# Optimization experiments

Measured on AMD Instinct MI355X. Metric: run time of the kernel, lower is better.

Reference implementation:

```python
import jax, jax.numpy as jnp
import numpy as np

V, WD, H, B, S, A = 50000, 300, 300, 64, 128, 8
H2 = 2 * H
NEG = -1e9


def _reverse_padded(x, lens):
    # reverse each sequence within its valid length; zeros elsewhere
    T = x.shape[1]
    idx = lens[:, None] - 1 - jnp.arange(T)[None, :]          # [B,T]
    valid = (idx >= 0)
    idx = jnp.clip(idx, 0, T - 1)
    return jnp.take_along_axis(x, idx[:, :, None], axis=1) * valid[:, :, None]


def _lstm_dir(x, lens, Wih, Whh, bih, bhh):
    # single-direction LSTM; emulates pack_padded: state frozen and output 0 past lens
    Bn, T, _ = x.shape
    Hn = Whh.shape[1]
    h0 = jnp.zeros((Bn, Hn), x.dtype)
    valid = (jnp.arange(T)[None, :] < lens[:, None]).astype(x.dtype)  # [B,T]

    def step(carry, inp):
        h, c = carry
        xt, vt = inp                                          # xt [B,D], vt [B,1]
        g = xt @ Wih.T + bih + h @ Whh.T + bhh                # [B,4H]
        i, f, gg, o = jnp.split(g, 4, axis=-1)                # torch gate order i,f,g,o
        i = jax.nn.sigmoid(i); f = jax.nn.sigmoid(f)
        o = jax.nn.sigmoid(o); gg = jnp.tanh(gg)
        c_new = f * c + i * gg
        h_new = o * jnp.tanh(c_new)
        h = vt * h_new + (1.0 - vt) * h
        c = vt * c_new + (1.0 - vt) * c
        return (h, c), vt * h_new

    _, outs = jax.lax.scan(step, (h0, h0), (x.transpose(1, 0, 2), valid.T[:, :, None]))
    return outs.transpose(1, 0, 2)                            # [B,T,H]


def _bilstm(x, lens, Wih, Whh, bih, bhh):
    fwd = _lstm_dir(x, lens, Wih[0], Whh[0], bih[0], bhh[0])
    xr = _reverse_padded(x, lens)
    bwd = _lstm_dir(xr, lens, Wih[1], Whh[1], bih[1], bhh[1])
    bwd = _reverse_padded(bwd, lens)
    return jnp.concatenate([fwd, bwd], axis=-1)               # [B,T,2H]


def setup_inputs() -> dict:
    key = jax.random.key(0)
    ks = jax.random.split(key, 16)
    lens_t = jax.random.randint(ks[0], (B,), S // 2, S + 1)
    ids_t = jax.random.randint(ks[1], (B, S), 1, V)
    text = jnp.where(jnp.arange(S)[None, :] < lens_t[:, None], ids_t, 0)
    lens_a = jax.random.randint(ks[2], (B,), 2, A + 1)
    ids_a = jax.random.randint(ks[3], (B, A), 1, V)
    aspect_ids = jnp.where(jnp.arange(A)[None, :] < lens_a[:, None], ids_a, 0)
    position_weight = jax.random.uniform(ks[4], (B, S), jnp.float32) * (text != 0)
    s = 0.05
    emb = jax.random.normal(ks[5], (V, WD), jnp.float32) * s
    emb = emb.at[0].set(0.0)  # padding row

    def lstm_params(k):
        k1, k2, k3, k4 = jax.random.split(k, 4)
        return (jax.random.normal(k1, (2, 4 * H, WD), jnp.float32) * s,
                jax.random.normal(k2, (2, 4 * H, H), jnp.float32) * s,
                jax.random.normal(k3, (2, 4 * H), jnp.float32) * s,
                jax.random.normal(k4, (2, 4 * H), jnp.float32) * s)

    l1_Wih, l1_Whh, l1_bih, l1_bhh = lstm_params(ks[6])
    l2_Wih, l2_Whh, l2_bih, l2_bhh = lstm_params(ks[7])
    return dict(
        text=text, aspect_ids=aspect_ids, position_weight=position_weight, emb=emb,
        l1_Wih=l1_Wih, l1_Whh=l1_Whh, l1_bih=l1_bih, l1_bhh=l1_bhh,
        l2_Wih=l2_Wih, l2_Whh=l2_Whh, l2_bih=l2_bih, l2_bhh=l2_bhh,
        lin1_W=jax.random.normal(ks[8], (2, H2, 2 * H2), jnp.float32) * s,
        lin1_b=jax.random.normal(ks[9], (2, H2), jnp.float32) * s,
        lin2_W=jax.random.normal(ks[10], (2, 1, H2), jnp.float32) * s,
        lin2_b=jax.random.normal(ks[11], (2, 1), jnp.float32) * s,
        fc_W=jax.random.normal(ks[12], (3, H2), jnp.float32) * s,
        fc_b=jax.random.normal(ks[13], (3,), jnp.float32) * s,
    )


def reference(text, aspect_ids, position_weight, emb,
              l1_Wih, l1_Whh, l1_bih, l1_bhh,
              l2_Wih, l2_Whh, l2_bih, l2_bhh,
              lin1_W, lin1_b, lin2_W, lin2_b, fc_W, fc_b):
    text_len = jnp.sum(text != 0, axis=-1)
    asp_len = jnp.sum(aspect_ids != 0, axis=-1)
    masks = (text != 0).astype(jnp.float32)          # [B,S]
    tmasks = (aspect_ids != 0).astype(jnp.float32)   # [B,A]
    wf = emb[text]                                    # [B,S,WD]
    af = emb[aspect_ids]                              # [B,A,WD]
    v = _bilstm(wf, text_len, l1_Wih, l1_Whh, l1_bih, l1_bhh)   # [B,S,2H]
    e = _bilstm(af, asp_len, l2_Wih, l2_Whh, l2_bih, l2_bhh)    # [B,A,2H]
    pair_mask = masks[:, :, None] * tmasks[:, None, :]          # [B,S,A]
    for i in range(2):
        a = jnp.einsum('bsd,bad->bsa', v, e)
        a = jnp.where(pair_mask == 0, NEG, a)
        a = jax.nn.softmax(a, axis=2)
        mid = jnp.einsum('bsa,bad->bsd', a, e)                  # [B,S,2H]
        mid = jnp.concatenate([mid, v], axis=-1)                # [B,S,4H]
        mid = jax.nn.leaky_relu(mid @ lin1_W[i].T + lin1_b[i])  # [B,S,2H]
        t = jax.nn.sigmoid(v @ lin2_W[i].T + lin2_b[i])         # [B,S,1]
        v = (1.0 - t) * mid + t * v
        v = position_weight[:, :, None] * v
    e_masked = jnp.where(tmasks[:, :, None] == 0, NEG, e)
    query = jnp.max(e_masked, axis=1)                           # [B,2H]
    alpha = jnp.einsum('bsd,bd->bs', v, query)
    alpha = jnp.where(masks == 0, NEG, alpha)
    alpha = jax.nn.softmax(alpha, axis=1)
    z = jnp.einsum('bs,bsd->bd', alpha, v)                      # [B,2H]
    return z @ fc_W.T + fc_b                                    # [B,3]
```

## Files before the change

### kernel.cpp

```cpp
#include <hip/hip_runtime.h>
#include <hip/hip_bf16.h>
#include <hip/hip_fp16.h>


typedef unsigned short u16;
typedef __attribute__((ext_vector_type(8))) short short8;
typedef __attribute__((ext_vector_type(4))) float floatx4;

#define NEGV -1e9f
#define MFMA __builtin_amdgcn_mfma_f32_16x16x32_bf16

__device__ __forceinline__ float bf2f(u16 u) {
    union { unsigned int i; float f; } x; x.i = ((unsigned int)u) << 16; return x.f;
}
__device__ __forceinline__ u16 f2bf(float f) {
    unsigned int u = __float_as_uint(f);
    unsigned int r = (u + 0x7fff + ((u >> 16) & 1)) >> 16;
    return (u16)r;
}
__device__ __forceinline__ float h16(u16 u) {
    __half h; *(u16*)&h = u; return __half2float(h);
}
__device__ __forceinline__ u16 f16(float f) {
    __half h = __float2half(f); return *(u16*)&h;
}
__device__ __forceinline__ float sigm(float x) { return 1.f / (1.f + expf(-x)); }
__device__ __forceinline__ float rdf(const void* p, size_t i, int flag) {
    return flag ? ((const float*)p)[i] : bf2f(((const u16*)p)[i]);
}

#if defined(__has_builtin)
# if __has_builtin(__builtin_amdgcn_fdot2)
#  define USE_FDOT2_BUILTIN 1
# endif
#endif
typedef __attribute__((ext_vector_type(2))) _Float16 half2v;
__device__ __forceinline__ float dot2f(unsigned int w, unsigned int h, float acc) {
#ifdef USE_FDOT2_BUILTIN
    union { unsigned int u; half2v v; } a, b;
    a.u = w; b.u = h;
    return __builtin_amdgcn_fdot2(a.v, b.v, acc, false);
#else
    asm("v_dot2_f32_f16 %0, %1, %2, %0" : "+v"(acc) : "v"(w), "v"(h));
    return acc;
#endif
}

__global__ void k_detect(const void* __restrict__ emb, int* __restrict__ flag) {
    __shared__ int cnt;
    if (threadIdx.x == 0) cnt = 0;
    __syncthreads();
    u16 x = ((const u16*)emb)[4096 + threadIdx.x];
    int e = (x >> 7) & 0xFF;
    if (e >= 0x8A) atomicAdd(&cnt, 1);
    __syncthreads();
    if (threadIdx.x == 0) *flag = (cnt > 8) ? 1 : 0;
}

__global__ void k_prep_small(const int* __restrict__ text, const int* __restrict__ asp,
                             int* __restrict__ lens) {
    int tid = threadIdx.x;
    if (tid < 64) {
        int c = 0;
        for (int s = 0; s < 128; ++s) c += (text[tid * 128 + s] != 0);
        lens[tid] = c;
    } else if (tid < 128) {
        int b = tid - 64; int c = 0;
        for (int a = 0; a < 8; ++a) c += (asp[b * 8 + a] != 0);
        lens[64 + b] = c;
    }
}

__global__ void k_pad_wih2(const void* __restrict__ W1, const void* __restrict__ W2,
                           const int* __restrict__ flag,
                           u16* __restrict__ d1h, u16* __restrict__ d1l,
                           u16* __restrict__ d2h, u16* __restrict__ d2l) {
    int i = blockIdx.x * 256 + threadIdx.x;
    if (i >= 2 * 2432 * 320) return;
    int f = *flag;
    int layer = i / (2432 * 320), r = i - layer * (2432 * 320);
    int n = r / 320, k = r - n * 320;
    const void* W = layer ? W2 : W1;
    float val = (n < 2400 && k < 300) ? rdf(W, (size_t)n * 300 + k, f) : 0.f;
    u16 hi = f2bf(val);
    float lo = val - bf2f(hi);
    if (layer) { d2h[r] = hi; d2l[r] = f2bf(lo); }
    else       { d1h[r] = hi; d1l[r] = f2bf(lo); }
}

__global__ void k_whhT2(const void* __restrict__ W1, const void* __restrict__ W2,
                        const int* __restrict__ flag,
                        u16* __restrict__ d1, u16* __restrict__ d2) {
    int i = blockIdx.x * 256 + threadIdx.x;
    if (i >= 2 * 720000) return;
    int f = *flag;
    int layer = i / 720000, r = i - layer * 720000;
    int dir = r / 360000, rr = r - dir * 360000;
    int kp = rr / 2400, t = rr - kp * 2400;
    int cc = t >> 1, j = t & 1;
    int k = 2 * kp + j;
    const void* W = layer ? W2 : W1;
    u16 bits = f16(rdf(W, (size_t)dir * 360000 + (size_t)cc * 300 + k, f));
    if (layer) d2[r] = bits; else d1[r] = bits;
}

__global__ void k_pad_lin1AB(const void* __restrict__ W, const int* __restrict__ flag,
                             u16* __restrict__ Ahi, u16* __restrict__ Alo,
                             u16* __restrict__ Bhi, u16* __restrict__ Blo) {
    int i = blockIdx.x * 256 + threadIdx.x;
    if (i >= 2 * 640 * 608) return;
    int f = *flag;
    int it = i / (640 * 608), r = i - it * (640 * 608);
    int n = r / 608, k = r - n * 608;
    float va = 0.f, vb = 0.f;
    if (n < 600 && k < 600) {
        va = rdf(W, (size_t)it * 720000 + (size_t)n * 1200 + k, f);
        vb = rdf(W, (size_t)it * 720000 + (size_t)n * 1200 + 600 + k, f);
    }
    u16 h;
    h = f2bf(va); Ahi[i] = h; Alo[i] = f2bf(va - bf2f(h));
    h = f2bf(vb); Bhi[i] = h; Blo[i] = f2bf(vb - bf2f(h));
}

__global__ void k_esplit(const float* __restrict__ e,
                         u16* __restrict__ ehi, u16* __restrict__ elo) {
    int i = blockIdx.x * 256 + threadIdx.x;
    if (i >= 512 * 608) return;
    int r = i / 608, k = i - r * 608;
    float val = (k < 600) ? e[r * 600 + k] : 0.f;
    u16 h = f2bf(val);
    ehi[i] = h;
    elo[i] = f2bf(val - bf2f(h));
}

__global__ void k_small(const void* pw, const void* l2w, const void* l2b,
                        const void* fcw, const void* fcb, const void* lb,
                        const void* b1i, const void* b1h, const void* b2i, const void* b2h,
                        const int* __restrict__ flag,
                        float* __restrict__ dst, float* __restrict__ bl,
                        float* __restrict__ bt, float* __restrict__ ba) {
    int i = blockIdx.x * 256 + threadIdx.x;
    int f = *flag;
    if (i < 8192)            dst[i] = rdf(pw, i, f);
    else if (i < 9392)       dst[i] = rdf(l2w, i - 8192, f);
    else if (i < 9394)       dst[i] = rdf(l2b, i - 9392, f);
    else if (i < 11194)      dst[i] = rdf(fcw, i - 9394, f);
    else if (i < 11197)      dst[i] = rdf(fcb, i - 11194, f);
    if (i < 1280) {
        int dir = i / 640, c = i - dir * 640;
        bl[i] = (c < 600) ? rdf(lb, dir * 600 + c, f) : 0.f;
    }
    if (i < 2400) {
        bt[i] = rdf(b1i, i, f) + rdf(b1h, i, f);
        ba[i] = rdf(b2i, i, f) + rdf(b2h, i, f);
    }
}

__device__ __forceinline__ void gemm_emb_tile(
    const void* __restrict__ emb, const int* __restrict__ ids,
    int base, int rpb, int stride, int f,
    const u16* __restrict__ Bhi, const u16* __restrict__ Blo,
    const float* __restrict__ bias,
    u16* __restrict__ C, int ldc, int nstore, int bx, int by, int tid)
{
    int wave = tid >> 6, lane = tid & 63;
    int l15 = lane & 15, quad = lane >> 4;
    int m0 = bx * 64 + wave * 16;
    int n0 = by * 64;

    int m = m0 + l15;
    int b = m / rpb, j = m - b * rpb;
    int id = ids[b * stride + base + j];
    const float* arow_f = (const float*)emb + (size_t)id * 300;
    const u16*   arow_b = (const u16*)emb + (size_t)id * 300;

    const u16* Bp  = Bhi + (size_t)(n0 + l15) * 320 + quad * 8;
    const u16* Bp2 = Blo + (size_t)(n0 + l15) * 320 + quad * 8;

    floatx4 acc0 = {0.f, 0.f, 0.f, 0.f};
    floatx4 acc1 = acc0, acc2 = acc0, acc3 = acc0;

    for (int kc = 0; kc < 10; ++kc) {
        int ko = kc * 32 + quad * 8;
        short8 ahi, alo;
        if (f) {
            if (ko + 8 <= 300) {
                float4 fa = *(const float4*)(arow_f + ko);
                float4 fb = *(const float4*)(arow_f + ko + 4);
                float vv[8] = {fa.x, fa.y, fa.z, fa.w, fb.x, fb.y, fb.z, fb.w};
                #pragma unroll
                for (int t = 0; t < 8; ++t) {
                    u16 h = f2bf(vv[t]);
                    ahi[t] = (short)h;
                    alo[t] = (short)f2bf(vv[t] - bf2f(h));
                }
            } else {
                #pragma unroll
                for (int t = 0; t < 8; ++t) {
                    int k = ko + t;
                    float vv = (k < 300) ? arow_f[k] : 0.f;
                    u16 h = f2bf(vv);
                    ahi[t] = (short)h;
                    alo[t] = (short)f2bf(vv - bf2f(h));
                }
            }
        } else {
            #pragma unroll
            for (int t = 0; t < 8; ++t) {
                int k = ko + t;
                ahi[t] = (k < 300) ? (short)arow_b[k] : (short)0;
                alo[t] = 0;
            }
        }
        int ko2 = kc * 32;
        short8 bh0 = *(const short8*)(Bp + ko2);
        short8 bh1 = *(const short8*)(Bp + (size_t)16 * 320 + ko2);
        short8 bh2 = *(const short8*)(Bp + (size_t)32 * 320 + ko2);
        short8 bh3 = *(const short8*)(Bp + (size_t)48 * 320 + ko2);
        short8 bl0 = *(const short8*)(Bp2 + ko2);
        short8 bl1 = *(const short8*)(Bp2 + (size_t)16 * 320 + ko2);
        short8 bl2 = *(const short8*)(Bp2 + (size_t)32 * 320 + ko2);
        short8 bl3 = *(const short8*)(Bp2 + (size_t)48 * 320 + ko2);
        acc0 = MFMA(ahi, bh0, acc0, 0, 0, 0);
        acc1 = MFMA(ahi, bh1, acc1, 0, 0, 0);
        acc2 = MFMA(ahi, bh2, acc2, 0, 0, 0);
        acc3 = MFMA(ahi, bh3, acc3, 0, 0, 0);
        acc0 = MFMA(ahi, bl0, acc0, 0, 0, 0);
        acc1 = MFMA(ahi, bl1, acc1, 0, 0, 0);
        acc2 = MFMA(ahi, bl2, acc2, 0, 0, 0);
        acc3 = MFMA(ahi, bl3, acc3, 0, 0, 0);
        acc0 = MFMA(alo, bh0, acc0, 0, 0, 0);
        acc1 = MFMA(alo, bh1, acc1, 0, 0, 0);
        acc2 = MFMA(alo, bh2, acc2, 0, 0, 0);
        acc3 = MFMA(alo, bh3, acc3, 0, 0, 0);
    }

    #pragma unroll
    for (int c = 0; c < 4; ++c) {
        floatx4 acc = (c == 0) ? acc0 : (c == 1) ? acc1 : (c == 2) ? acc2 : acc3;
        int col = n0 + c * 16 + l15;
        if (col >= nstore) continue;
        float bb = bias[col];
        #pragma unroll
        for (int r = 0; r < 4; ++r) {
            int row = m0 + quad * 4 + r;
            C[(size_t)row * ldc + col] = f16(acc[r] + bb);
        }
    }
}

__global__ __launch_bounds__(256) void gemm_embk(
    const void* __restrict__ emb, const int* __restrict__ ids,
    int base, int rpb, int stride, const int* __restrict__ flag,
    const u16* __restrict__ Bhi, const u16* __restrict__ Blo,
    const float* __restrict__ bias,
    u16* __restrict__ C, int ldc, int nstore)
{
    gemm_emb_tile(emb, ids, base, rpb, stride, *flag, Bhi, Blo, bias,
                  C, ldc, nstore, blockIdx.x, blockIdx.y, threadIdx.x);
}

__device__ __forceinline__ void gemm_core(
    const u16* __restrict__ Ap, const u16* __restrict__ Ap2,
    const u16* __restrict__ Bp, const u16* __restrict__ Bp2,
    int lda, int ldb, int nk,
    floatx4& acc0, floatx4& acc1, floatx4& acc2, floatx4& acc3)
{
    for (int kc = 0; kc < nk; ++kc) {
        int ko = kc * 32;
        short8 bh0 = *(const short8*)(Bp + ko);
        short8 bh1 = *(const short8*)(Bp + (size_t)16 * ldb + ko);
        short8 bh2 = *(const short8*)(Bp + (size_t)32 * ldb + ko);
        short8 bh3 = *(const short8*)(Bp + (size_t)48 * ldb + ko);
        short8 bl0 = *(const short8*)(Bp2 + ko);
        short8 bl1 = *(const short8*)(Bp2 + (size_t)16 * ldb + ko);
        short8 bl2 = *(const short8*)(Bp2 + (size_t)32 * ldb + ko);
        short8 bl3 = *(const short8*)(Bp2 + (size_t)48 * ldb + ko);
        short8 a  = *(const short8*)(Ap + ko);
        short8 al = *(const short8*)(Ap2 + ko);
        acc0 = MFMA(a, bh0, acc0, 0, 0, 0);
        acc1 = MFMA(a, bh1, acc1, 0, 0, 0);
        acc2 = MFMA(a, bh2, acc2, 0, 0, 0);
        acc3 = MFMA(a, bh3, acc3, 0, 0, 0);
        acc0 = MFMA(a, bl0, acc0, 0, 0, 0);
        acc1 = MFMA(a, bl1, acc1, 0, 0, 0);
        acc2 = MFMA(a, bl2, acc2, 0, 0, 0);
        acc3 = MFMA(a, bl3, acc3, 0, 0, 0);
        acc0 = MFMA(al, bh0, acc0, 0, 0, 0);
        acc1 = MFMA(al, bh1, acc1, 0, 0, 0);
        acc2 = MFMA(al, bh2, acc2, 0, 0, 0);
        acc3 = MFMA(al, bh3, acc3, 0, 0, 0);
    }
}

__global__ __launch_bounds__(256) void gemm_ew(
    const u16* __restrict__ Ahi, const u16* __restrict__ Alo,
    const u16* __restrict__ l1a_hi, const u16* __restrict__ l1a_lo,
    float* __restrict__ EW)
{
    int tid = threadIdx.x;
    int wave = tid >> 6, lane = tid & 63;
    int l15 = lane & 15, quad = lane >> 4;
    int iter = blockIdx.z;
    int m0 = blockIdx.x * 64 + wave * 16;
    int n0 = blockIdx.y * 64;
    const u16* Ap  = Ahi + (size_t)(m0 + l15) * 608 + quad * 8;
    const u16* Ap2 = Alo + (size_t)(m0 + l15) * 608 + quad * 8;
    const u16* Bp  = l1a_hi + (size_t)iter * 640 * 608 + (size_t)(n0 + l15) * 608 + quad * 8;
    const u16* Bp2 = l1a_lo + (size_t)iter * 640 * 608 + (size_t)(n0 + l15) * 608 + quad * 8;
    floatx4 acc0 = {0.f, 0.f, 0.f, 0.f};
    floatx4 acc1 = acc0, acc2 = acc0, acc3 = acc0;
    gemm_core(Ap, Ap2, Bp, Bp2, 608, 608, 19, acc0, acc1, acc2, acc3);
    #pragma unroll
    for (int c = 0; c < 4; ++c) {
        floatx4 acc = (c == 0) ? acc0 : (c == 1) ? acc1 : (c == 2) ? acc2 : acc3;
        int col = n0 + c * 16 + l15;
        if (col >= 600) continue;
        #pragma unroll
        for (int r = 0; r < 4; ++r) {
            int row = m0 + quad * 4 + r;
            EW[((size_t)iter * 512 + row) * 600 + col] = acc[r];
        }
    }
}

__global__ __launch_bounds__(256) void gemm_vt(
    const u16* __restrict__ vhi, const u16* __restrict__ vlo,
    const u16* __restrict__ Bhi, const u16* __restrict__ Blo,
    const float* __restrict__ bias,
    const float* __restrict__ EW, const float* __restrict__ a_sm,
    const float* __restrict__ tg, const float* __restrict__ pw,
    float* __restrict__ vio)
{
    __shared__ float al_s[64][8];
    __shared__ float ew_s[8][64];
    int tid = threadIdx.x;
    int wave = tid >> 6, lane = tid & 63;
    int l15 = lane & 15, quad = lane >> 4;
    int m0 = blockIdx.x * 64 + wave * 16;
    int n0 = blockIdx.y * 64;
    int row0 = blockIdx.x * 64;
    int bidx = row0 >> 7;

    for (int i = tid; i < 512; i += 256)
        al_s[i >> 3][i & 7] = a_sm[(size_t)(row0 + (i >> 3)) * 8 + (i & 7)];
    for (int i = tid; i < 512; i += 256) {
        int a = i >> 6, cc = i & 63;
        int col = n0 + cc;
        ew_s[a][cc] = (col < 600) ? EW[((size_t)bidx * 8 + a) * 600 + col] : 0.f;
    }
    __syncthreads();

    const u16* Ap  = vhi + (size_t)(m0 + l15) * 608 + quad * 8;
    const u16* Ap2 = vlo + (size_t)(m0 + l15) * 608 + quad * 8;
    const u16* Bp  = Bhi + (size_t)(n0 + l15) * 608 + quad * 8;
    const u16* Bp2 = Blo + (size_t)(n0 + l15) * 608 + quad * 8;
    floatx4 acc0 = {0.f, 0.f, 0.f, 0.f};
    floatx4 acc1 = acc0, acc2 = acc0, acc3 = acc0;
    gemm_core(Ap, Ap2, Bp, Bp2, 608, 608, 19, acc0, acc1, acc2, acc3);

    #pragma unroll
    for (int c = 0; c < 4; ++c) {
        floatx4 acc = (c == 0) ? acc0 : (c == 1) ? acc1 : (c == 2) ? acc2 : acc3;
        int cc = c * 16 + l15;
        int col = n0 + cc;
        if (col >= 600) continue;
        float bb = bias[col];
        #pragma unroll
        for (int r = 0; r < 4; ++r) {
            int rr = wave * 16 + quad * 4 + r;
            int row = row0 + rr;
            float mid = 0.f;
            #pragma unroll
            for (int a = 0; a < 8; ++a) mid += al_s[rr][a] * ew_s[a][cc];
            float val = acc[r] + bb + mid;
            val = val > 0.f ? val : 0.01f * val;
            float t = tg[row];
            size_t vi = (size_t)row * 600 + col;
            float vv = vio[vi];
            vio[vi] = pw[row] * ((1.f - t) * val + t * vv);
        }
    }
}

__global__ __launch_bounds__(960, 1) void k_lstm6(
    const u16* __restrict__ xf, const u16* __restrict__ xb, int ldx, int rpb,
    int base_f, int base_b, const u16* __restrict__ whhT,
    const int* __restrict__ lens, float* __restrict__ out, int T, int init,
    float* __restrict__ hst, float* __restrict__ cst, int nsteps,
    const u16* __restrict__ xa, const u16* __restrict__ whhA,
    const int* __restrict__ lensA, float* __restrict__ outA,
    float* __restrict__ hstA, float* __restrict__ cstA, int nLstm,
    const void* __restrict__ emb, const int* __restrict__ text,
    int bf_next, int bb_next, const int* __restrict__ flag,
    const u16* __restrict__ wih_hi, const u16* __restrict__ wih_lo,
    const float* __restrict__ bias_t,
    u16* __restrict__ xf_next, u16* __restrict__ xb_next)
{
    __shared__ float part[6][1200];
    __shared__ u16 wlds[6][4][2400];
    __shared__ __align__(4) u16 hs16[304];
    int blk = blockIdx.x;
    if (blk >= nLstm) {
        if (threadIdx.x >= 256) return;
        int g = blk - nLstm;
        int dirn = g / 608; int t = g - dirn * 608;
        int bx = t & 31, by = t >> 5;
        gemm_emb_tile(emb, text, dirn ? bb_next : bf_next, 32, 128, *flag,
                      wih_hi + (dirn ? 1200ull * 320 : 0),
                      wih_lo + (dirn ? 1200ull * 320 : 0),
                      bias_t + (dirn ? 1200 : 0),
                      dirn ? xb_next : xf_next, 1200, 1200, bx, by, threadIdx.x);
        return;
    }
    if (blk >= 128) {
        blk -= 128;
        xf = xa; xb = xa + 1200; ldx = 2400; rpb = 8;
        base_f = 0; base_b = 0;
        whhT = whhA; lens = lensA; out = outA; T = 8; init = 1;
        hst = hstA; cst = cstA; nsteps = 8;
    }
    int tid = threadIdx.x;
    int g6 = tid / 160, u = tid - g6 * 160;
    bool act = (u < 150);
    int b = blk >> 1, dir = blk & 1;
    int len = lens[b];
    float c = 0.f, hf = 0.f;
    const u16* wbase = whhT + (size_t)dir * 360000 + (size_t)g6 * 60000 + 16 * u;

    uint4 wA[8], wB[8];
    if (act) {
        #pragma unroll
        for (int r = 0; r < 8; ++r) {
            wA[r] = *(const uint4*)(wbase + (size_t)r * 2400);
            wB[r] = *(const uint4*)(wbase + (size_t)r * 2400 + 8);
        }
        #pragma unroll
        for (int r = 0; r < 4; ++r) {
            *(uint4*)&wlds[g6][r][16 * u]     = *(const uint4*)(wbase + (size_t)(8 + r) * 2400);
            *(uint4*)&wlds[g6][r][16 * u + 8] = *(const uint4*)(wbase + (size_t)(8 + r) * 2400 + 8);
        }
    }
    if (tid < 300) {
        hf = init ? 0.f : hst[(size_t)blk * 300 + tid];
        c  = init ? 0.f : cst[(size_t)blk * 300 + tid];
        hs16[tid] = f16(hf);
    }
    __syncthreads();
    const u16* wstream = wbase + (size_t)12 * 2400;

    for (int s = 0; s < nsteps; ++s) {
        int pos = dir ? (base_b + nsteps - 1 - s) : (base_f + s);
        if (pos >= len) continue;
        if (act) {
            float a0 = 0.f, a1 = 0.f, a2 = 0.f, a3 = 0.f;
            float a4 = 0.f, a5 = 0.f, a6 = 0.f, a7 = 0.f;
            const unsigned int* h2p = (const unsigned int*)(hs16 + g6 * 50);
            #define DOT8(va, vb, hh)                                   \
                a0 = dot2f((va).x, hh, a0); a1 = dot2f((va).y, hh, a1);\
                a2 = dot2f((va).z, hh, a2); a3 = dot2f((va).w, hh, a3);\
                a4 = dot2f((vb).x, hh, a4); a5 = dot2f((vb).y, hh, a5);\
                a6 = dot2f((vb).z, hh, a6); a7 = dot2f((vb).w, hh, a7);
            #pragma unroll
            for (int r = 0; r < 8; ++r) {
                unsigned int h2 = h2p[r];
                DOT8(wA[r], wB[r], h2);
            }
            #pragma unroll
            for (int r = 0; r < 4; ++r) {
                unsigned int h2 = h2p[8 + r];
                uint4 va = *(const uint4*)&wlds[g6][r][16 * u];
                uint4 vb = *(const uint4*)&wlds[g6][r][16 * u + 8];
                DOT8(va, vb, h2);
            }
            const u16* wp = wstream;
            #pragma unroll 4
            for (int i = 0; i < 13; ++i) {
                unsigned int h2 = h2p[12 + i];
                uint4 va = *(const uint4*)wp;
                uint4 vb = *(const uint4*)(wp + 8);
                wp += 2400;
                DOT8(va, vb, h2);
            }
            #undef DOT8
            float* pp = &part[g6][8 * u];
            float4 w0 = {a0, a1, a2, a3};
            float4 w1 = {a4, a5, a6, a7};
            *(float4*)pp = w0;
            *(float4*)(pp + 4) = w1;
        }
        __syncthreads();
        if (tid < 300) {
            const u16* xr = dir ? (xb + (size_t)(b * rpb + pos - base_b) * ldx)
                                : (xf + (size_t)(b * rpb + pos - base_f) * ldx);
            float gi = h16(xr[tid]), gf = h16(xr[300 + tid]);
            float gg = h16(xr[600 + tid]), go = h16(xr[900 + tid]);
            #pragma unroll
            for (int g = 0; g < 6; ++g) {
                gi += part[g][tid];
                gf += part[g][300 + tid];
                gg += part[g][600 + tid];
                go += part[g][900 + tid];
            }
            gi = sigm(gi); gf = sigm(gf); gg = tanhf(gg); go = sigm(go);
            c = gf * c + gi * gg;
            float hn = go * tanhf(c);
            out[((size_t)b * T + pos) * 600 + dir * 300 + tid] = hn;
            hf = hn;
            hs16[tid] = f16(hn);
        }
        __syncthreads();
    }
    if (tid < 300) {
        hst[(size_t)blk * 300 + tid] = hf;
        cst[(size_t)blk * 300 + tid] = c;
    }
}

__global__ __launch_bounds__(128) void k_scorev(
    const float* __restrict__ v, const float* __restrict__ e,
    const int* __restrict__ text, const int* __restrict__ asp,
    const float* __restrict__ l2w, const float* __restrict__ l2b, int iter,
    float* __restrict__ a_sm, float* __restrict__ tg,
    u16* __restrict__ vhi, u16* __restrict__ vlo)
{
    __shared__ float vs[600];
    __shared__ float red[2][9];
    int row = blockIdx.x;
    int b = row >> 7;
    int t = threadIdx.x, wv = t >> 6, lane = t & 63;
    const float* vrow = v + (size_t)row * 600;
    const float* eb = e + (size_t)b * 4800;
    const float* w2 = l2w + iter * 600;

    for (int d = t; d < 600; d += 128) vs[d] = vrow[d];
    __syncthreads();

    float acc[9];
    #pragma unroll
    for (int j = 0; j < 9; ++j) acc[j] = 0.f;
    for (int d = t; d < 600; d += 128) {
        float vv = vs[d];
        #pragma unroll
        for (int a = 0; a < 8; ++a) acc[a] += vv * eb[a * 600 + d];
        acc[8] += vv * w2[d];
    }
    #pragma unroll
    for (int off = 32; off >= 1; off >>= 1) {
        #pragma unroll
        for (int j = 0; j < 9; ++j) acc[j] += __shfl_down(acc[j], off, 64);
    }
    if (lane == 0) {
        #pragma unroll
        for (int j = 0; j < 9; ++j) red[wv][j] = acc[j];
    }
    __syncthreads();
    if (t == 0) {
        float dots[9];
        #pragma unroll
        for (int j = 0; j < 9; ++j) dots[j] = red[0][j] + red[1][j];
        tg[row] = sigm(dots[8] + l2b[iter]);
        bool sm = (text[row] != 0);
        float sc[8]; float mx = -INFINITY;
        #pragma unroll
        for (int a = 0; a < 8; ++a) {
            sc[a] = (sm && asp[b * 8 + a] != 0) ? dots[a] : NEGV;
            mx = fmaxf(mx, sc[a]);
        }
        float den = 0.f;
        #pragma unroll
        for (int a = 0; a < 8; ++a) { sc[a] = expf(sc[a] - mx); den += sc[a]; }
        float inv = 1.f / den;
        #pragma unroll
        for (int a = 0; a < 8; ++a) a_sm[(size_t)row * 8 + a] = sc[a] * inv;
    }
    for (int d = t; d < 608; d += 128) {
        float val = (d < 600) ? vs[d] : 0.f;
        u16 h = f2bf(val);
        vhi[(size_t)row * 608 + d] = h;
        vlo[(size_t)row * 608 + d] = f2bf(val - bf2f(h));
    }
}

__global__ void k_query(const float* __restrict__ e, const int* __restrict__ asp,
                        float* __restrict__ q) {
    int i = blockIdx.x * 256 + threadIdx.x;
    if (i >= 64 * 600) return;
    int b = i / 600, d = i - b * 600;
    float m = NEGV;
    for (int a = 0; a < 8; ++a)
        if (asp[b * 8 + a] != 0) m = fmaxf(m, e[(size_t)b * 4800 + a * 600 + d]);
    q[i] = m;
}

__global__ __launch_bounds__(128) void k_final(
    const float* __restrict__ v, const float* __restrict__ q,
    const int* __restrict__ text, const float* __restrict__ fcW,
    const float* __restrict__ fcb, const int* __restrict__ flag, void* __restrict__ outv)
{
    __shared__ float red[128];
    __shared__ float al[128];
    __shared__ float zz[600];
    int b = blockIdx.x, s = threadIdx.x;
    const float* vrow = v + (size_t)(b * 128 + s) * 600;
    const float* qb = q + (size_t)b * 600;
    float sc = 0.f;
    for (int d = 0; d < 600; ++d) sc += vrow[d] * qb[d];
    if (text[b * 128 + s] == 0) sc = NEGV;
    red[s] = sc; __syncthreads();
    for (int off = 64; off >= 1; off >>= 1) {
        if (s < off) red[s] = fmaxf(red[s], red[s + off]);
        __syncthreads();
    }
    float mx = red[0]; __syncthreads();
    float ex = expf(sc - mx);
    red[s] = ex; __syncthreads();
    for (int off = 64; off >= 1; off >>= 1) {
        if (s < off) red[s] += red[s + off];
        __syncthreads();
    }
    float alpha = ex / red[0];
    al[s] = alpha; __syncthreads();
    for (int d = s; d < 600; d += 128) {
        float z = 0.f;
        for (int s2 = 0; s2 < 128; ++s2) z += al[s2] * v[(size_t)(b * 128 + s2) * 600 + d];
        zz[d] = z;
    }
    __syncthreads();
    if (s < 3) {
        float o = 0.f;
        for (int d = 0; d < 600; ++d) o += zz[d] * fcW[s * 600 + d];
        o += fcb[s];
        if (*flag) ((float*)outv)[b * 3 + s] = o;
        else       ((u16*)outv)[b * 3 + s] = f2bf(o);
    }
}

extern "C" void kernel_launch(void* const* d_in, const int* in_sizes, int n_in,
                              void* d_out, int out_size, void* d_ws, size_t ws_size,
                              hipStream_t stream) {
    const int*  text   = (const int*)d_in[0];
    const int*  asp    = (const int*)d_in[1];
    const void* pw     = d_in[2];
    const void* emb    = d_in[3];
    const void* l1_Wih = d_in[4];
    const void* l1_Whh = d_in[5];
    const void* l1_bih = d_in[6];
    const void* l1_bhh = d_in[7];
    const void* l2_Wih = d_in[8];
    const void* l2_Whh = d_in[9];
    const void* l2_bih = d_in[10];
    const void* l2_bhh = d_in[11];
    const void* lin1_W = d_in[12];
    const void* lin1_b = d_in[13];
    const void* lin2_W = d_in[14];
    const void* lin2_b = d_in[15];
    const void* fcW    = d_in[16];
    const void* fcb    = d_in[17];
    (void)ws_size; (void)n_in; (void)in_sizes; (void)out_size;

    char* w = (char*)d_ws;
    size_t off = 0;
    auto alloc = [&](size_t bytes) -> void* {
        void* p = w + off;
        off += (bytes + 255) & ~(size_t)255;
        return p;
    };
    int*   flag     = (int*)  alloc(4);
    int*   lens     = (int*)  alloc(128ull * 4);
    float* bias_t   = (float*)alloc(2400ull * 4);
    float* bias_a   = (float*)alloc(2400ull * 4);
    float* bias_l1  = (float*)alloc(1280ull * 4);
    float* smallf   = (float*)alloc(11197ull * 4);
    float* tg       = (float*)alloc(8192ull * 4);
    float* a_sm     = (float*)alloc(8192ull * 8 * 4);
    float* query    = (float*)alloc(64ull * 600 * 4);
    float* hst_t    = (float*)alloc(128ull * 300 * 4);
    float* cst_t    = (float*)alloc(128ull * 300 * 4);
    float* hst_a    = (float*)alloc(128ull * 300 * 4);
    float* cst_a    = (float*)alloc(128ull * 300 * 4);
    float* e        = (float*)alloc(512ull * 600 * 4);
    float* v        = (float*)alloc(8192ull * 600 * 4);
    float* pw_f     = smallf;
    float* l2w_f    = smallf + 8192;
    float* l2b_f    = smallf + 9392;
    float* fcW_f    = smallf + 9394;
    float* fcb_f    = smallf + 11194;
    size_t phase_off = off;
    u16*   wiht_hi  = (u16*)  alloc(2432ull * 320 * 2);
    u16*   wiht_lo  = (u16*)  alloc(2432ull * 320 * 2);
    u16*   wiha_hi  = (u16*)  alloc(2432ull * 320 * 2);
    u16*   wiha_lo  = (u16*)  alloc(2432ull * 320 * 2);
    u16*   whhT_t   = (u16*)  alloc(720000ull * 2);
    u16*   whhT_a   = (u16*)  alloc(720000ull * 2);
    u16*   xf0      = (u16*)  alloc(2048ull * 1200 * 2);
    u16*   xb0      = (u16*)  alloc(2048ull * 1200 * 2);
    u16*   xf1      = (u16*)  alloc(2048ull * 1200 * 2);
    u16*   xb1      = (u16*)  alloc(2048ull * 1200 * 2);
    u16*   xproj_a  = (u16*)  alloc(512ull * 2400 * 2);
    off = phase_off;
    u16*   l1a_hi   = (u16*)  alloc(2ull * 640 * 608 * 2);
    u16*   l1a_lo   = (u16*)  alloc(2ull * 640 * 608 * 2);
    u16*   l1b_hi   = (u16*)  alloc(2ull * 640 * 608 * 2);
    u16*   l1b_lo   = (u16*)  alloc(2ull * 640 * 608 * 2);
    u16*   ehi      = (u16*)  alloc(512ull * 608 * 2);
    u16*   elo      = (u16*)  alloc(512ull * 608 * 2);
    float* EW       = (float*)alloc(2ull * 512 * 600 * 4);
    u16*   vhi      = (u16*)  alloc(8192ull * 608 * 2);
    u16*   vlo      = (u16*)  alloc(8192ull * 608 * 2);

    hipMemsetAsync(v, 0, 8192ull * 600 * 4, stream);
    hipMemsetAsync(e, 0, 512ull * 600 * 4, stream);

    k_detect<<<1, 256, 0, stream>>>(emb, flag);
    k_prep_small<<<1, 128, 0, stream>>>(text, asp, lens);
    k_pad_wih2<<<(2 * 2432 * 320 + 255) / 256, 256, 0, stream>>>(
        l1_Wih, l2_Wih, flag, wiht_hi, wiht_lo, wiha_hi, wiha_lo);
    k_whhT2<<<(2 * 720000 + 255) / 256, 256, 0, stream>>>(
        l1_Whh, l2_Whh, flag, whhT_t, whhT_a);
    k_small<<<49, 256, 0, stream>>>(pw, lin2_W, lin2_b, fcW, fcb, lin1_b,
                                    l1_bih, l1_bhh, l2_bih, l2_bhh, flag,
                                    smallf, bias_l1, bias_t, bias_a);

    gemm_embk<<<dim3(8, 38), 256, 0, stream>>>(emb, asp, 0, 8, 8, flag,
        wiha_hi, wiha_lo, bias_a, xproj_a, 2400, 2400);
    gemm_embk<<<dim3(32, 19), 256, 0, stream>>>(emb, text, 0, 32, 128, flag,
        wiht_hi, wiht_lo, bias_t, xf0, 1200, 1200);
    gemm_embk<<<dim3(32, 19), 256, 0, stream>>>(emb, text, 96, 32, 128, flag,
        wiht_hi + 1200ull * 320, wiht_lo + 1200ull * 320, bias_t + 1200,
        xb0, 1200, 1200);

    for (int kk = 0; kk < 4; ++kk) {
        int bf = 32 * kk;
        int bb = 96 - 32 * kk;
        u16* xfc = (kk & 1) ? xf1 : xf0;
        u16* xbc = (kk & 1) ? xb1 : xb0;
        u16* xfn = (kk & 1) ? xf0 : xf1;
        u16* xbn = (kk & 1) ? xb0 : xb1;
        int nLstm = (kk == 0) ? 256 : 128;
        int haveNext = (kk < 3);
        int nblk = nLstm + (haveNext ? 1216 : 0);
        k_lstm6<<<nblk, 960, 0, stream>>>(xfc, xbc, 1200, 32, bf, bb,
            whhT_t, lens, v, 128, kk == 0 ? 1 : 0, hst_t, cst_t, 32,
            xproj_a, whhT_a, lens + 64, e, hst_a, cst_a, nLstm,
            emb, text, bf + 32, bb - 32, flag, wiht_hi, wiht_lo, bias_t,
            xfn, xbn);
    }

    k_pad_lin1AB<<<(2 * 640 * 608 + 255) / 256, 256, 0, stream>>>(
        lin1_W, flag, l1a_hi, l1a_lo, l1b_hi, l1b_lo);
    k_esplit<<<(512 * 608 + 255) / 256, 256, 0, stream>>>(e, ehi, elo);
    gemm_ew<<<dim3(8, 10, 2), 256, 0, stream>>>(ehi, elo, l1a_hi, l1a_lo, EW);

    for (int iter = 0; iter < 2; ++iter) {
        k_scorev<<<8192, 128, 0, stream>>>(v, e, text, asp, l2w_f, l2b_f,
            iter, a_sm, tg, vhi, vlo);
        gemm_vt<<<dim3(128, 10), 256, 0, stream>>>(vhi, vlo,
            l1b_hi + (size_t)iter * 640 * 608, l1b_lo + (size_t)iter * 640 * 608,
            bias_l1 + iter * 640, EW + (size_t)iter * 512 * 600,
            a_sm, tg, pw_f, v);
    }

    k_query<<<150, 256, 0, stream>>>(e, asp, query);
    k_final<<<64, 128, 0, stream>>>(v, query, text, fcW_f, fcb_f, flag, d_out);
}
```

Measured before the change: 1.102 ms.

## Merge prep kernels and fold query/lin1 padding into LSTM launches

Folds the weight-prep kernels into one large launch, merges the three embedding GEMMs into one grid, and appends the query max-reduction and lin1 weight padding as extra blocks of the LSTM chunk launches. The aim is to cut kernel launch count and fill idle CUs during the latency-bound LSTM recurrence. k_final also stages v tiles through shared memory so the per-row dot product reads coalesced. The risk is that the extra 960-thread blocks compete with the LSTM blocks for CUs. The query blocks run in the kk==1 launch and read the aspect outputs, which depends on the aspect LSTM having finished in an earlier chunk.

```diff
diff --git a/kernel.cpp b/kernel.cpp
--- a/kernel.cpp
+++ b/kernel.cpp
@@ -57,102 +57,68 @@
     if (threadIdx.x == 0) *flag = (cnt > 8) ? 1 : 0;
 }
 
-__global__ void k_prep_small(const int* __restrict__ text, const int* __restrict__ asp,
-                             int* __restrict__ lens) {
+__global__ __launch_bounds__(256) void k_prep_all(
+    const int* __restrict__ text, const int* __restrict__ asp,
+    int* __restrict__ lens, const int* __restrict__ flag,
+    const void* __restrict__ W1ih, const void* __restrict__ W2ih,
+    u16* __restrict__ d1h, u16* __restrict__ d1l,
+    u16* __restrict__ d2h, u16* __restrict__ d2l,
+    const void* __restrict__ W1hh, const void* __restrict__ W2hh,
+    u16* __restrict__ dh1, u16* __restrict__ dh2,
+    const void* pw, const void* l2w, const void* l2b,
+    const void* fcw, const void* fcb, const void* lb,
+    const void* b1i, const void* b1h, const void* b2i, const void* b2h,
+    float* __restrict__ dst, float* __restrict__ bl,
+    float* __restrict__ bt, float* __restrict__ ba)
+{
+    int blk = blockIdx.x;
     int tid = threadIdx.x;
-    if (tid < 64) {
-        int c = 0;
-        for (int s = 0; s < 128; ++s) c += (text[tid * 128 + s] != 0);
-        lens[tid] = c;
-    } else if (tid < 128) {
-        int b = tid - 64; int c = 0;
-        for (int a = 0; a < 8; ++a) c += (asp[b * 8 + a] != 0);
-        lens[64 + b] = c;
-    }
-}
-
-__global__ void k_pad_wih2(const void* __restrict__ W1, const void* __restrict__ W2,
-                           const int* __restrict__ flag,
-                           u16* __restrict__ d1h, u16* __restrict__ d1l,
-                           u16* __restrict__ d2h, u16* __restrict__ d2l) {
-    int i = blockIdx.x * 256 + threadIdx.x;
-    if (i >= 2 * 2432 * 320) return;
     int f = *flag;
-    int layer = i / (2432 * 320), r = i - layer * (2432 * 320);
-    int n = r / 320, k = r - n * 320;
-    const void* W = layer ? W2 : W1;
-    float val = (n < 2400 && k < 300) ? rdf(W, (size_t)n * 300 + k, f) : 0.f;
-    u16 hi = f2bf(val);
-    float lo = val - bf2f(hi);
-    if (layer) { d2h[r] = hi; d2l[r] = f2bf(lo); }
-    else       { d1h[r] = hi; d1l[r] = f2bf(lo); }
-}
-
-__global__ void k_whhT2(const void* __restrict__ W1, const void* __restrict__ W2,
-                        const int* __restrict__ flag,
-                        u16* __restrict__ d1, u16* __restrict__ d2) {
-    int i = blockIdx.x * 256 + threadIdx.x;
-    if (i >= 2 * 720000) return;
-    int f = *flag;
-    int layer = i / 720000, r = i - layer * 720000;
-    int dir = r / 360000, rr = r - dir * 360000;
-    int kp = rr / 2400, t = rr - kp * 2400;
-    int cc = t >> 1, j = t & 1;
-    int k = 2 * kp + j;
-    const void* W = layer ? W2 : W1;
-    u16 bits = f16(rdf(W, (size_t)dir * 360000 + (size_t)cc * 300 + k, f));
-    if (layer) d2[r] = bits; else d1[r] = bits;
-}
-
-__global__ void k_pad_lin1AB(const void* __restrict__ W, const int* __restrict__ flag,
-                             u16* __restrict__ Ahi, u16* __restrict__ Alo,
-                             u16* __restrict__ Bhi, u16* __restrict__ Blo) {
-    int i = blockIdx.x * 256 + threadIdx.x;
-    if (i >= 2 * 640 * 608) return;
-    int f = *flag;
-    int it = i / (640 * 608), r = i - it * (640 * 608);
-    int n = r / 608, k = r - n * 608;
-    float va = 0.f, vb = 0.f;
-    if (n < 600 && k < 600) {
-        va = rdf(W, (size_t)it * 720000 + (size_t)n * 1200 + k, f);
-        vb = rdf(W, (size_t)it * 720000 + (size_t)n * 1200 + 600 + k, f);
-    }
-    u16 h;
-    h = f2bf(va); Ahi[i] = h; Alo[i] = f2bf(va - bf2f(h));
-    h = f2bf(vb); Bhi[i] = h; Blo[i] = f2bf(vb - bf2f(h));
-}
-
-__global__ void k_esplit(const float* __restrict__ e,
-                         u16* __restrict__ ehi, u16* __restrict__ elo) {
-    int i = blockIdx.x * 256 + threadIdx.x;
-    if (i >= 512 * 608) return;
-    int r = i / 608, k = i - r * 608;
-    float val = (k < 600) ? e[r * 600 + k] : 0.f;
-    u16 h = f2bf(val);
-    ehi[i] = h;
-    elo[i] = f2bf(val - bf2f(h));
-}
-
-__global__ void k_small(const void* pw, const void* l2w, const void* l2b,
-                        const void* fcw, const void* fcb, const void* lb,
-                        const void* b1i, const void* b1h, const void* b2i, const void* b2h,
-                        const int* __restrict__ flag,
-                        float* __restrict__ dst, float* __restrict__ bl,
-                        float* __restrict__ bt, float* __restrict__ ba) {
-    int i = blockIdx.x * 256 + threadIdx.x;
-    int f = *flag;
-    if (i < 8192)            dst[i] = rdf(pw, i, f);
-    else if (i < 9392)       dst[i] = rdf(l2w, i - 8192, f);
-    else if (i < 9394)       dst[i] = rdf(l2b, i - 9392, f);
-    else if (i < 11194)      dst[i] = rdf(fcw, i - 9394, f);
-    else if (i < 11197)      dst[i] = rdf(fcb, i - 11194, f);
-    if (i < 1280) {
-        int dir = i / 640, c = i - dir * 640;
-        bl[i] = (c < 600) ? rdf(lb, dir * 600 + c, f) : 0.f;
-    }
-    if (i < 2400) {
-        bt[i] = rdf(b1i, i, f) + rdf(b1h, i, f);
-        ba[i] = rdf(b2i, i, f) + rdf(b2h, i, f);
+    if (blk < 6080) {
+        int i = blk * 256 + tid;
+        int layer = i / (2432 * 320), r = i - layer * (2432 * 320);
+        int n = r / 320, k = r - n * 320;
+        const void* W = layer ? W2ih : W1ih;
+        float val = (n < 2400 && k < 300) ? rdf(W, (size_t)n * 300 + k, f) : 0.f;
+        u16 hi = f2bf(val);
+        float lo = val - bf2f(hi);
+        if (layer) { d2h[r] = hi; d2l[r] = f2bf(lo); }
+        else       { d1h[r] = hi; d1l[r] = f2bf(lo); }
+    } else if (blk < 11705) {
+        int i = (blk - 6080) * 256 + tid;
+        int layer = i / 720000, r = i - layer * 720000;
+        int dir = r / 360000, rr = r - dir * 360000;
+        int kp = rr / 2400, t = rr - kp * 2400;
+        int cc = t >> 1, j = t & 1;
+        int k = 2 * kp + j;
+        const void* W = layer ? W2hh : W1hh;
+        u16 bits = f16(rdf(W, (size_t)dir * 360000 + (size_t)cc * 300 + k, f));
+        if (layer) dh2[r] = bits; else dh1[r] = bits;
+    } else if (blk < 11754) {
+        int i = (blk - 11705) * 256 + tid;
+        if (i < 8192)            dst[i] = rdf(pw, i, f);
+        else if (i < 9392)       dst[i] = rdf(l2w, i - 8192, f);
+        else if (i < 9394)       dst[i] = rdf(l2b, i - 9392, f);
+        else if (i < 11194)      dst[i] = rdf(fcw, i - 9394, f);
+        else if (i < 11197)      dst[i] = rdf(fcb, i - 11194, f);
+        if (i < 1280) {
+            int dir = i / 640, c = i - dir * 640;
+            bl[i] = (c < 600) ? rdf(lb, dir * 600 + c, f) : 0.f;
+        }
+        if (i < 2400) {
+            bt[i] = rdf(b1i, i, f) + rdf(b1h, i, f);
+            ba[i] = rdf(b2i, i, f) + rdf(b2h, i, f);
+        }
+    } else {
+        if (tid < 64) {
+            int c = 0;
+            for (int s = 0; s < 128; ++s) c += (text[tid * 128 + s] != 0);
+            lens[tid] = c;
+        } else if (tid < 128) {
+            int b = tid - 64; int c = 0;
+            for (int a = 0; a < 8; ++a) c += (asp[b * 8 + a] != 0);
+            lens[64 + b] = c;
+        }
     }
 }
 
@@ -249,15 +215,30 @@
     }
 }
 
-__global__ __launch_bounds__(256) void gemm_embk(
-    const void* __restrict__ emb, const int* __restrict__ ids,
-    int base, int rpb, int stride, const int* __restrict__ flag,
-    const u16* __restrict__ Bhi, const u16* __restrict__ Blo,
-    const float* __restrict__ bias,
-    u16* __restrict__ C, int ldc, int nstore)
-{
-    gemm_emb_tile(emb, ids, base, rpb, stride, *flag, Bhi, Blo, bias,
-                  C, ldc, nstore, blockIdx.x, blockIdx.y, threadIdx.x);
+__global__ __launch_bounds__(256) void k_gemm_emb3(
+    const void* __restrict__ emb, const int* __restrict__ text,
+    const int* __restrict__ asp, const int* __restrict__ flag,
+    const u16* __restrict__ wiht_hi, const u16* __restrict__ wiht_lo,
+    const u16* __restrict__ wiha_hi, const u16* __restrict__ wiha_lo,
+    const float* __restrict__ bias_t, const float* __restrict__ bias_a,
+    u16* __restrict__ xproj_a, u16* __restrict__ xf0, u16* __restrict__ xb0)
+{
+    int g = blockIdx.x;
+    int f = *flag;
+    if (g < 304) {
+        int bx = g & 7, by = g >> 3;
+        gemm_emb_tile(emb, asp, 0, 8, 8, f, wiha_hi, wiha_lo, bias_a,
+                      xproj_a, 2400, 2400, bx, by, threadIdx.x);
+    } else if (g < 912) {
+        int t = g - 304; int bx = t & 31, by = t >> 5;
+        gemm_emb_tile(emb, text, 0, 32, 128, f, wiht_hi, wiht_lo, bias_t,
+                      xf0, 1200, 1200, bx, by, threadIdx.x);
+    } else {
+        int t = g - 912; int bx = t & 31, by = t >> 5;
+        gemm_emb_tile(emb, text, 96, 32, 128, f,
+                      wiht_hi + 1200ull * 320, wiht_lo + 1200ull * 320,
+                      bias_t + 1200, xb0, 1200, 1200, bx, by, threadIdx.x);
+    }
 }
 
 __device__ __forceinline__ void gemm_core(
@@ -293,6 +274,17 @@
     }
 }
 
+__global__ void k_esplit(const float* __restrict__ e,
+                         u16* __restrict__ ehi, u16* __restrict__ elo) {
+    int i = blockIdx.x * 256 + threadIdx.x;
+    if (i >= 512 * 608) return;
+    int r = i / 608, k = i - r * 608;
+    float val = (k < 600) ? e[r * 600 + k] : 0.f;
+    u16 h = f2bf(val);
+    ehi[i] = h;
+    elo[i] = f2bf(val - bf2f(h));
+}
+
 __global__ __launch_bounds__(256) void gemm_ew(
     const u16* __restrict__ Ahi, const u16* __restrict__ Alo,
     const u16* __restrict__ l1a_hi, const u16* __restrict__ l1a_lo,
@@ -395,12 +387,45 @@
     int bf_next, int bb_next, const int* __restrict__ flag,
     const u16* __restrict__ wih_hi, const u16* __restrict__ wih_lo,
     const float* __restrict__ bias_t,
-    u16* __restrict__ xf_next, u16* __restrict__ xb_next)
+    u16* __restrict__ xf_next, u16* __restrict__ xb_next,
+    int nGemm, int fmode, const int* __restrict__ aspF,
+    float* __restrict__ queryF, const void* __restrict__ lin1W,
+    u16* __restrict__ l1a_hi, u16* __restrict__ l1a_lo,
+    u16* __restrict__ l1b_hi, u16* __restrict__ l1b_lo)
 {
     __shared__ float part[6][1200];
     __shared__ u16 wlds[6][4][2400];
     __shared__ __align__(4) u16 hs16[304];
     int blk = blockIdx.x;
+    if (blk >= nLstm + nGemm) {
+        int fb = blk - nLstm - nGemm;
+        int i = fb * 960 + threadIdx.x;
+        if (fmode == 1) {
+            if (i < 64 * 600) {
+                int b = i / 600, d = i - b * 600;
+                float m = NEGV;
+                for (int a = 0; a < 8; ++a)
+                    if (aspF[b * 8 + a] != 0)
+                        m = fmaxf(m, outA[(size_t)b * 4800 + a * 600 + d]);
+                queryF[i] = m;
+            }
+        } else {
+            if (i < 2 * 640 * 608) {
+                int f = *flag;
+                int it = i / (640 * 608), r = i - it * (640 * 608);
+                int n = r / 608, k = r - n * 608;
+                float va = 0.f, vb = 0.f;
+                if (n < 600 && k < 600) {
+                    va = rdf(lin1W, (size_t)it * 720000 + (size_t)n * 1200 + k, f);
+                    vb = rdf(lin1W, (size_t)it * 720000 + (size_t)n * 1200 + 600 + k, f);
+                }
+                u16 h;
+                h = f2bf(va); l1a_hi[i] = h; l1a_lo[i] = f2bf(va - bf2f(h));
+                h = f2bf(vb); l1b_hi[i] = h; l1b_lo[i] = f2bf(vb - bf2f(h));
+            }
+        }
+        return;
+    }
     if (blk >= nLstm) {
         if (threadIdx.x >= 256) return;
         int g = blk - nLstm;
@@ -582,17 +607,6 @@
     }
 }
 
-__global__ void k_query(const float* __restrict__ e, const int* __restrict__ asp,
-                        float* __restrict__ q) {
-    int i = blockIdx.x * 256 + threadIdx.x;
-    if (i >= 64 * 600) return;
-    int b = i / 600, d = i - b * 600;
-    float m = NEGV;
-    for (int a = 0; a < 8; ++a)
-        if (asp[b * 8 + a] != 0) m = fmaxf(m, e[(size_t)b * 4800 + a * 600 + d]);
-    q[i] = m;
-}
-
 __global__ __launch_bounds__(128) void k_final(
     const float* __restrict__ v, const float* __restrict__ q,
     const int* __restrict__ text, const float* __restrict__ fcW,
@@ -601,11 +615,29 @@
     __shared__ float red[128];
     __shared__ float al[128];
     __shared__ float zz[600];
+    __shared__ float qs[608];
+    __shared__ float vt[128][33];
     int b = blockIdx.x, s = threadIdx.x;
-    const float* vrow = v + (size_t)(b * 128 + s) * 600;
-    const float* qb = q + (size_t)b * 600;
+    const float* vb = v + (size_t)b * 128 * 600;
+    for (int d = s; d < 608; d += 128) qs[d] = (d < 600) ? q[(size_t)b * 600 + d] : 0.f;
+    __syncthreads();
     float sc = 0.f;
-    for (int d = 0; d < 600; ++d) sc += vrow[d] * qb[d];
+    for (int d0 = 0; d0 < 600; d0 += 32) {
+        #pragma unroll
+        for (int k = 0; k < 4; ++k) {
+            ;
+        }
+        for (int i = s; i < 128 * 32; i += 128) {
+            int row = i >> 5, col = i & 31;
+            int d = d0 + col;
+            vt[row][col] = (d < 600) ? vb[(size_t)row * 600 + d] : 0.f;
+        }
+        __syncthreads();
+        #pragma unroll
+        for (int col = 0; col < 32; ++col)
+            sc += vt[s][col] * qs[d0 + col];
+        __syncthreads();
+    }
     if (text[b * 128 + s] == 0) sc = NEGV;
     red[s] = sc; __syncthreads();
     for (int off = 64; off >= 1; off >>= 1) {
@@ -713,22 +745,17 @@
     hipMemsetAsync(e, 0, 512ull * 600 * 4, stream);
 
     k_detect<<<1, 256, 0, stream>>>(emb, flag);
-    k_prep_small<<<1, 128, 0, stream>>>(text, asp, lens);
-    k_pad_wih2<<<(2 * 2432 * 320 + 255) / 256, 256, 0, stream>>>(
-        l1_Wih, l2_Wih, flag, wiht_hi, wiht_lo, wiha_hi, wiha_lo);
-    k_whhT2<<<(2 * 720000 + 255) / 256, 256, 0, stream>>>(
-        l1_Whh, l2_Whh, flag, whhT_t, whhT_a);
-    k_small<<<49, 256, 0, stream>>>(pw, lin2_W, lin2_b, fcW, fcb, lin1_b,
-                                    l1_bih, l1_bhh, l2_bih, l2_bhh, flag,
-                                    smallf, bias_l1, bias_t, bias_a);
-
-    gemm_embk<<<dim3(8, 38), 256, 0, stream>>>(emb, asp, 0, 8, 8, flag,
-        wiha_hi, wiha_lo, bias_a, xproj_a, 2400, 2400);
-    gemm_embk<<<dim3(32, 19), 256, 0, stream>>>(emb, text, 0, 32, 128, flag,
-        wiht_hi, wiht_lo, bias_t, xf0, 1200, 1200);
-    gemm_embk<<<dim3(32, 19), 256, 0, stream>>>(emb, text, 96, 32, 128, flag,
-        wiht_hi + 1200ull * 320, wiht_lo + 1200ull * 320, bias_t + 1200,
-        xb0, 1200, 1200);
+    k_prep_all<<<11755, 256, 0, stream>>>(
+        text, asp, lens, flag,
+        l1_Wih, l2_Wih, wiht_hi, wiht_lo, wiha_hi, wiha_lo,
+        l1_Whh, l2_Whh, whhT_t, whhT_a,
+        pw, lin2_W, lin2_b, fcW, fcb, lin1_b,
+        l1_bih, l1_bhh, l2_bih, l2_bhh,
+        smallf, bias_l1, bias_t, bias_a);
+
+    k_gemm_emb3<<<1520, 256, 0, stream>>>(
+        emb, text, asp, flag, wiht_hi, wiht_lo, wiha_hi, wiha_lo,
+        bias_t, bias_a, xproj_a, xf0, xb0);
 
     for (int kk = 0; kk < 4; ++kk) {
         int bf = 32 * kk;
@@ -738,17 +765,19 @@
         u16* xfn = (kk & 1) ? xf0 : xf1;
         u16* xbn = (kk & 1) ? xb0 : xb1;
         int nLstm = (kk == 0) ? 256 : 128;
-        int haveNext = (kk < 3);
-        int nblk = nLstm + (haveNext ? 1216 : 0);
+        int nGemm = (kk < 3) ? 1216 : 0;
+        int fmode = (kk == 1) ? 1 : (kk == 3) ? 2 : 0;
+        int nFuse = (kk == 1) ? 40 : (kk == 3) ? 811 : 0;
+        int nblk = nLstm + nGemm + nFuse;
         k_lstm6<<<nblk, 960, 0, stream>>>(xfc, xbc, 1200, 32, bf, bb,
             whhT_t, lens, v, 128, kk == 0 ? 1 : 0, hst_t, cst_t, 32,
             xproj_a, whhT_a, lens + 64, e, hst_a, cst_a, nLstm,
             emb, text, bf + 32, bb - 32, flag, wiht_hi, wiht_lo, bias_t,
-            xfn, xbn);
-    }
-
-    k_pad_lin1AB<<<(2 * 640 * 608 + 255) / 256, 256, 0, stream>>>(
-        lin1_W, flag, l1a_hi, l1a_lo, l1b_hi, l1b_lo);
+            xfn, xbn,
+            nGemm, fmode, asp, query, lin1_W,
+            l1a_hi, l1a_lo, l1b_hi, l1b_lo);
+    }
+
     k_esplit<<<(512 * 608 + 255) / 256, 256, 0, stream>>>(e, ehi, elo);
     gemm_ew<<<dim3(8, 10, 2), 256, 0, stream>>>(ehi, elo, l1a_hi, l1a_lo, EW);
 
@@ -761,6 +790,5 @@
             a_sm, tg, pw_f, v);
     }
 
-    k_query<<<150, 256, 0, stream>>>(e, asp, query);
     k_final<<<64, 128, 0, stream>>>(v, query, text, fcW_f, fcb_f, flag, d_out);
 }
```

After: 1.208 ms. +9.6%, slower.
